# Performance work log

Measured on AMD Instinct MI355X. Metric: run time of the kernel, lower is better.

The kernel has to match this reference:

```python
import jax, jax.numpy as jnp
import numpy as np

N_NODES = 50000
E_DIM = 128
H_DIM = 256
OUT_DIM = 2
N_EDGES = 800000
NEG_SLOPE = 0.01  # nn.LeakyReLU default


def gcn_conv(x, W, b, src, dst, n):
    """PyG GCNConv: h = x @ W; add self-loops; sym-normalized scatter-add; + bias."""
    h = x @ W  # [N, H]
    loop = jnp.arange(n, dtype=src.dtype)
    s = jnp.concatenate([src, loop])
    d = jnp.concatenate([dst, loop])
    w = jnp.ones_like(s, dtype=h.dtype)
    deg = jax.ops.segment_sum(w, d, num_segments=n)  # in-degree incl. self-loop
    dis = jnp.where(deg > 0, jax.lax.rsqrt(deg), jnp.zeros_like(deg))
    norm = dis[s] * dis[d]  # [E+N]
    msg = h[s] * norm[:, None]  # gather + scale
    out = jax.ops.segment_sum(msg, d, num_segments=n)  # scatter-add to targets
    return out + b


def setup_inputs() -> dict:
    key = jax.random.key(0)
    ks = jax.random.split(key, 12)
    inp = {
        "mask_feature": jax.random.normal(ks[0], (N_NODES, E_DIM), jnp.float32),
        "feature": jax.random.normal(ks[1], (N_NODES, E_DIM), jnp.float32),
        "edge_index": jax.random.randint(ks[2], (2, N_EDGES), 0, N_NODES, jnp.int64 if jax.config.jax_enable_x64 else jnp.int32),
        "edge_type": jax.random.randint(ks[3], (N_EDGES,), 0, 2, jnp.int64 if jax.config.jax_enable_x64 else jnp.int32),
        # learned parameters
        "W_in": jax.random.normal(ks[4], (E_DIM, H_DIM), jnp.float32) * 0.05,
        "b_in": jnp.zeros((H_DIM,), jnp.float32),
        "Wg1": jax.random.normal(ks[5], (H_DIM, H_DIM), jnp.float32) * 0.05,
        "bg1": jnp.zeros((H_DIM,), jnp.float32),
        "Wg2": jax.random.normal(ks[6], (H_DIM, H_DIM), jnp.float32) * 0.05,
        "bg2": jnp.zeros((H_DIM,), jnp.float32),
        "W_out": jax.random.normal(ks[7], (H_DIM, OUT_DIM), jnp.float32) * 0.05,
        "b_out": jnp.zeros((OUT_DIM,), jnp.float32),
    }
    return inp


def reference(mask_feature, feature, edge_index, edge_type,
              W_in, b_in, Wg1, bg1, Wg2, bg2, W_out, b_out):
    src, dst = edge_index[0], edge_index[1]
    n = mask_feature.shape[0]
    # main branch
    x = jax.nn.leaky_relu(mask_feature @ W_in + b_in, NEG_SLOPE)
    x = gcn_conv(x, Wg1, bg1, src, dst, n)
    # dropout is identity at inference
    x = gcn_conv(x, Wg2, bg2, src, dst, n)
    x = x @ W_out + b_out  # [N, out_dim]
    # mask branch
    m = jax.nn.leaky_relu((feature - mask_feature) @ W_in + b_in, NEG_SLOPE)
    m = m @ W_out + b_out  # [N, out_dim]
    return x * m
```

## Files before the change

kernel.cpp:

```cpp
#include <hip/hip_runtime.h>


#define NEG_SLOPE 0.01f
constexpr int HD = 256;
constexpr int CHUNK = 4096;
constexpr int BSTRIDE = 8192;

typedef __bf16 bf16x8 __attribute__((ext_vector_type(8)));
typedef unsigned short u16x8 __attribute__((ext_vector_type(8)));
typedef float f32x4 __attribute__((ext_vector_type(4)));

#define MFMA16 __builtin_amdgcn_mfma_f32_16x16x32_bf16

__device__ inline void split1(float v, unsigned short& h, unsigned short& l) {
  unsigned u = __float_as_uint(v);
  unsigned hb = u & 0xFFFF0000u;
  float lf = v - __uint_as_float(hb);
  unsigned ul = __float_as_uint(lf);
  h = (unsigned short)(hb >> 16);
  l = (unsigned short)((ul + 0x7FFFu + ((ul >> 16) & 1u)) >> 16);
}

__global__ __launch_bounds__(256) void k_prep(
    const float* __restrict__ Win, u16x8* __restrict__ Wf,
    const float* __restrict__ Wg1, const float* __restrict__ Wg2,
    const float* __restrict__ Wo, const float* __restrict__ bg1,
    const float* __restrict__ bg2, const float* __restrict__ bo,
    float* __restrict__ wb, float* __restrict__ uv, int* __restrict__ cur) {
  __shared__ float wt[256][2];
  const int bid = blockIdx.x, tid = threadIdx.x;
  if (bid < 32) {
    int f = bid * 4 + (tid >> 6);
    int lane = tid & 63;
    int nt = f >> 3, ks = (f >> 1) & 3, hl = f & 1;
    int n = nt * 16 + (lane & 15);
    int k0 = ks * 32 + (lane >> 4) * 8;
    u16x8 outv;
    #pragma unroll
    for (int j = 0; j < 8; ++j) {
      unsigned short h, l;
      split1(Win[(size_t)(k0 + j) * HD + n], h, l);
      outv[j] = hl ? l : h;
    }
    Wf[f * 64 + lane] = outv;
  } else if (bid == 32) {
    int r = tid;
    float s0 = 0.f, s1 = 0.f;
    for (int k = 0; k < 256; ++k) {
      float w = Wg2[r * 256 + k];
      s0 = fmaf(w, Wo[k * 2 + 0], s0);
      s1 = fmaf(w, Wo[k * 2 + 1], s1);
    }
    wt[r][0] = s0; wt[r][1] = s1;
    __syncthreads();
    float b0 = 0.f, b1 = 0.f;
    for (int k = 0; k < 256; ++k) {
      float w = Wg1[r * 256 + k];
      b0 = fmaf(w, wt[k][0], b0);
      b1 = fmaf(w, wt[k][1], b1);
    }
    wb[r * 2 + 0] = b0; wb[r * 2 + 1] = b1;
    if (r < 2) {
      float u = 0.f, v = 0.f;
      for (int k = 0; k < 256; ++k) {
        u = fmaf(bg1[k], wt[k][r], u);
        v = fmaf(bg2[k], Wo[k * 2 + r], v);
      }
      uv[r] = u;
      uv[2 + r] = v + bo[r];
    }
  } else {
    cur[tid] = 0;
  }
}

__global__ __launch_bounds__(256) void k_scatter(
    const int* __restrict__ src, const int* __restrict__ dst,
    int* __restrict__ cur, unsigned* __restrict__ packed, int E) {
  __shared__ int bins[256], lstart[256], gbase[256], lcur[256];
  __shared__ int wsum[4];
  __shared__ unsigned sbuf[CHUNK];
  const int t = threadIdx.x, b = blockIdx.x;
  const int lane = t & 63, wid = t >> 6;
  bins[t] = 0;
  __syncthreads();
  const int e0 = b * CHUNK, e1 = min(e0 + CHUNK, E), m = e1 - e0;
  for (int e = e0 + t; e < e1; e += 256)
    atomicAdd(&bins[dst[e] >> 8], 1);
  __syncthreads();
  {
    int v = bins[t], incl = v;
    #pragma unroll
    for (int o = 1; o < 64; o <<= 1) {
      int tmp = __shfl_up(incl, o, 64);
      if (lane >= o) incl += tmp;
    }
    if (lane == 63) wsum[wid] = incl;
    __syncthreads();
    int woff = 0;
    for (int w = 0; w < wid; ++w) woff += wsum[w];
    int st = woff + incl - v;
    lstart[t] = st;
    lcur[t] = st;
    gbase[t] = v ? atomicAdd(&cur[t], v) : 0;
  }
  __syncthreads();
  for (int e = e0 + t; e < e1; e += 256) {
    int d = dst[e], s = src[e];
    int slot = atomicAdd(&lcur[d >> 8], 1);
    sbuf[slot] = ((unsigned)d << 16) | (unsigned)s;
  }
  __syncthreads();
  for (int i = t; i < m; i += 256) {
    unsigned pv = sbuf[i];
    int bin = pv >> 24;
    packed[(size_t)bin * BSTRIDE + gbase[bin] + (i - lstart[bin])] = pv;
  }
}

__global__ __launch_bounds__(256, 3) void k_main(
    const float* __restrict__ mf, const float* __restrict__ fe,
    const u16x8* __restrict__ Wf, const float* __restrict__ bi,
    const float* __restrict__ wb, const float* __restrict__ Wo,
    const float* __restrict__ bo, float4* __restrict__ q, float* __restrict__ Pm,
    const unsigned* __restrict__ packed, const int* __restrict__ cur,
    int* __restrict__ rp, int* __restrict__ csr, int N, int Gg) {
  __shared__ __align__(16) char smem[38912];
  const int tid = threadIdx.x;
  const int lane = tid & 63, wid = tid >> 6;

  if ((int)blockIdx.x < Gg) {
    u16x8*  sB  = (u16x8*)smem;
    float4* sE1 = (float4*)(smem + 32768);
    float2* sE2 = (float2*)(smem + 36864);
    sE1[tid] = make_float4(bi[tid], wb[2 * tid], wb[2 * tid + 1], 0.f);
    sE2[tid] = make_float2(Wo[2 * tid], Wo[2 * tid + 1]);

    const int base = blockIdx.x * 64 + wid * 16;
    int arow = base + (lane & 15);
    if (arow >= N) arow = N - 1;
    const int kb = (lane >> 4) * 8;
    const float* ap = mf + (size_t)arow * 128 + kb;
    const float* fp = fe + (size_t)arow * 128 + kb;

    bf16x8 ahi[4], alo[4], mhi[4], mlo[4];
    #pragma unroll
    for (int ks = 0; ks < 4; ++ks) {
      float x[8], y[8];
      *(float4*)&x[0] = *(const float4*)(ap + ks * 32);
      *(float4*)&x[4] = *(const float4*)(ap + ks * 32 + 4);
      *(float4*)&y[0] = *(const float4*)(fp + ks * 32);
      *(float4*)&y[4] = *(const float4*)(fp + ks * 32 + 4);
      u16x8 hA, lA, hM, lM;
      #pragma unroll
      for (int j = 0; j < 8; ++j) {
        unsigned short hh, ll;
        split1(x[j], hh, ll);        hA[j] = hh; lA[j] = ll;
        split1(y[j] - x[j], hh, ll); hM[j] = hh; lM[j] = ll;
      }
      ahi[ks] = __builtin_bit_cast(bf16x8, hA);
      alo[ks] = __builtin_bit_cast(bf16x8, lA);
      mhi[ks] = __builtin_bit_cast(bf16x8, hM);
      mlo[ks] = __builtin_bit_cast(bf16x8, lM);
    }

    float s0[4] = {}, s1[4] = {}, t0[4] = {}, t1[4] = {};
    #pragma unroll 1
    for (int g = 0; g < 4; ++g) {
      __syncthreads();
      #pragma unroll
      for (int i = 0; i < 8; ++i)
        sB[tid + i * 256] = Wf[g * 2048 + tid + i * 256];
      __syncthreads();
      #pragma unroll
      for (int ntl = 0; ntl < 4; ++ntl) {
        const int nt = g * 4 + ntl;
        f32x4 aM = {0, 0, 0, 0}, aK = {0, 0, 0, 0};
        #pragma unroll
        for (int ks = 0; ks < 4; ++ks) {
          bf16x8 bh = __builtin_bit_cast(bf16x8, sB[(ntl * 8 + ks * 2 + 0) * 64 + lane]);
          bf16x8 bl = __builtin_bit_cast(bf16x8, sB[(ntl * 8 + ks * 2 + 1) * 64 + lane]);
          aM = MFMA16(ahi[ks], bh, aM, 0, 0, 0);
          aM = MFMA16(alo[ks], bh, aM, 0, 0, 0);
          aM = MFMA16(ahi[ks], bl, aM, 0, 0, 0);
          aK = MFMA16(mhi[ks], bh, aK, 0, 0, 0);
          aK = MFMA16(mlo[ks], bh, aK, 0, 0, 0);
          aK = MFMA16(mhi[ks], bl, aK, 0, 0, 0);
        }
        const int col = nt * 16 + (lane & 15);
        const float4 e1 = sE1[col];
        const float2 e2 = sE2[col];
        #pragma unroll
        for (int r = 0; r < 4; ++r) {
          float a = aM[r] + e1.x; a = a > 0.f ? a : NEG_SLOPE * a;
          s0[r] = fmaf(a, e1.y, s0[r]); s1[r] = fmaf(a, e1.z, s1[r]);
          float m = aK[r] + e1.x; m = m > 0.f ? m : NEG_SLOPE * m;
          t0[r] = fmaf(m, e2.x, t0[r]); t1[r] = fmaf(m, e2.y, t1[r]);
        }
      }
    }

    #pragma unroll
    for (int o = 1; o < 16; o <<= 1) {
      #pragma unroll
      for (int r = 0; r < 4; ++r) {
        s0[r] += __shfl_xor(s0[r], o, 16); s1[r] += __shfl_xor(s1[r], o, 16);
        t0[r] += __shfl_xor(t0[r], o, 16); t1[r] += __shfl_xor(t1[r], o, 16);
      }
    }
    if ((lane & 15) == 0) {
      float bo0 = bo[0], bo1 = bo[1];
      #pragma unroll
      for (int r = 0; r < 4; ++r) {
        int row = base + (lane >> 4) * 4 + r;
        if (row < N) {
          float* qf = (float*)&q[row];
          qf[1] = s0[r];
          qf[2] = s1[r];
          Pm[row * 2 + 0] = t0[r] + bo0;
          Pm[row * 2 + 1] = t1[r] + bo1;
        }
      }
    }
    return;
  }

  int* cnt = (int*)smem;
  int* sc  = (int*)(smem + 1024);
  int* wsum = (int*)(smem + 2048);
  unsigned short* sbuf = (unsigned short*)(smem + 2064);
  const int t = tid;
  const int B = blockIdx.x - Gg;
  int tot = cur[t], incl = tot;
  #pragma unroll
  for (int o = 1; o < 64; o <<= 1) {
    int tmp = __shfl_up(incl, o, 64);
    if (lane >= o) incl += tmp;
  }
  if (lane == 63) wsum[wid] = incl;
  __syncthreads();
  int woff = 0;
  for (int w = 0; w < wid; ++w) woff += wsum[w];
  sc[t] = woff + incl - tot;
  __syncthreads();
  const int base = sc[B];
  const int ecnt = cur[B];
  const unsigned* pk = packed + (size_t)B * BSTRIDE;
  cnt[t] = 0;
  __syncthreads();
  for (int i = t; i < ecnt; i += 256)
    atomicAdd(&cnt[(pk[i] >> 16) & 0xFF], 1);
  __syncthreads();
  int v = cnt[t];
  incl = v;
  #pragma unroll
  for (int o = 1; o < 64; o <<= 1) {
    int tmp = __shfl_up(incl, o, 64);
    if (lane >= o) incl += tmp;
  }
  if (lane == 63) wsum[wid] = incl;
  __syncthreads();
  woff = 0;
  for (int w = 0; w < wid; ++w) woff += wsum[w];
  const int off = woff + incl - v;
  const int node = B * 256 + t;
  if (node < N) {
    rp[node] = base + off;
    ((float*)&q[node])[0] = rsqrtf((float)(v + 1));
  } else if (node == N) {
    rp[N] = base + off;
  }
  __syncthreads();
  cnt[t] = off;
  __syncthreads();
  for (int i = t; i < ecnt; i += 256) {
    unsigned pv = pk[i];
    int slot = atomicAdd(&cnt[(pv >> 16) & 0xFF], 1);
    sbuf[slot] = (unsigned short)(pv & 0xFFFFu);
  }
  __syncthreads();
  for (int i = t; i < ecnt; i += 256)
    csr[base + i] = (int)sbuf[i];
}

__global__ __launch_bounds__(256) void k_gather1(
    const int* __restrict__ rp, const int* __restrict__ csr,
    const float4* __restrict__ q, const float* __restrict__ uv,
    float* __restrict__ T2, int N) {
  int t = threadIdx.x;
  int n = blockIdx.x * 64 + (t >> 2);
  int l = t & 3;
  if (n >= N) return;
  int s0 = rp[n], s1 = rp[n + 1];
  float a0 = 0.f, a1 = 0.f;
  int j = s0 + l;
  for (; j + 12 < s1; j += 16) {
    int i0 = csr[j], i1 = csr[j + 4], i2 = csr[j + 8], i3 = csr[j + 12];
    float4 q0 = q[i0], q1 = q[i1], q2 = q[i2], q3 = q[i3];
    a0 = fmaf(q0.x, q0.y, a0); a1 = fmaf(q0.x, q0.z, a1);
    a0 = fmaf(q1.x, q1.y, a0); a1 = fmaf(q1.x, q1.z, a1);
    a0 = fmaf(q2.x, q2.y, a0); a1 = fmaf(q2.x, q2.z, a1);
    a0 = fmaf(q3.x, q3.y, a0); a1 = fmaf(q3.x, q3.z, a1);
  }
  for (; j < s1; j += 4) {
    float4 qa = q[csr[j]];
    a0 = fmaf(qa.x, qa.y, a0); a1 = fmaf(qa.x, qa.z, a1);
  }
  a0 += __shfl_xor(a0, 1, 4); a1 += __shfl_xor(a1, 1, 4);
  a0 += __shfl_xor(a0, 2, 4); a1 += __shfl_xor(a1, 2, 4);
  if (l == 0) {
    float4 qn = q[n];
    float d = qn.x;
    T2[n * 2 + 0] = d * (d * fmaf(d, qn.y, a0) + uv[0]);
    T2[n * 2 + 1] = d * (d * fmaf(d, qn.z, a1) + uv[1]);
  }
}

__global__ __launch_bounds__(256) void k_gather2(
    const int* __restrict__ rp, const int* __restrict__ csr,
    const float* __restrict__ T2, const float4* __restrict__ q,
    const float* __restrict__ uv, const float* __restrict__ Pm,
    float* __restrict__ out, int N) {
  int t = threadIdx.x;
  int n = blockIdx.x * 64 + (t >> 2);
  int l = t & 3;
  if (n >= N) return;
  int s0 = rp[n], s1 = rp[n + 1];
  float a0 = 0.f, a1 = 0.f;
  int j = s0 + l;
  for (; j + 12 < s1; j += 16) {
    int i0 = csr[j], i1 = csr[j + 4], i2 = csr[j + 8], i3 = csr[j + 12];
    float2 v0 = *(const float2*)&T2[i0 * 2];
    float2 v1 = *(const float2*)&T2[i1 * 2];
    float2 v2 = *(const float2*)&T2[i2 * 2];
    float2 v3 = *(const float2*)&T2[i3 * 2];
    a0 += (v0.x + v1.x) + (v2.x + v3.x);
    a1 += (v0.y + v1.y) + (v2.y + v3.y);
  }
  for (; j < s1; j += 4) {
    float2 va = *(const float2*)&T2[csr[j] * 2];
    a0 += va.x; a1 += va.y;
  }
  a0 += __shfl_xor(a0, 1, 4); a1 += __shfl_xor(a1, 1, 4);
  a0 += __shfl_xor(a0, 2, 4); a1 += __shfl_xor(a1, 2, 4);
  if (l == 0) {
    float d = q[n].x;
    float2 tv = *(const float2*)&T2[n * 2];
    float z0 = d * (tv.x + a0) + uv[2];
    float z1 = d * (tv.y + a1) + uv[3];
    out[n * 2 + 0] = z0 * Pm[n * 2 + 0];
    out[n * 2 + 1] = z1 * Pm[n * 2 + 1];
  }
}

extern "C" void kernel_launch(void* const* d_in, const int* in_sizes, int n_in,
                              void* d_out, int out_size, void* d_ws, size_t ws_size,
                              hipStream_t stream) {
  const float* mf  = (const float*)d_in[0];
  const float* fe  = (const float*)d_in[1];
  const int*   ei  = (const int*)d_in[2];
  const float* Win = (const float*)d_in[4];
  const float* bin = (const float*)d_in[5];
  const float* Wg1 = (const float*)d_in[6];
  const float* bg1 = (const float*)d_in[7];
  const float* Wg2 = (const float*)d_in[8];
  const float* bg2 = (const float*)d_in[9];
  const float* Wo  = (const float*)d_in[10];
  const float* bo  = (const float*)d_in[11];
  float* out = (float*)d_out;

  const int ED = 128;
  const int N = in_sizes[0] / ED;
  const int E = in_sizes[3];
  const int* src = ei;
  const int* dst = ei + E;

  char* ws = (char*)d_ws;
  size_t off = 0;
  auto carve = [&](size_t bytes) {
    char* p = ws + off;
    off += (bytes + 255) & ~(size_t)255;
    return p;
  };
  int*      cur    = (int*)carve(256 * 4);
  unsigned* packed = (unsigned*)carve((size_t)256 * BSTRIDE * 4);
  int*      csr    = (int*)carve((size_t)E * 4);
  int*      rp     = (int*)carve((size_t)(N + 1) * 4);
  float4*   q      = (float4*)carve((size_t)N * 16);
  float*    T2     = (float*)carve((size_t)N * 2 * 4);
  float*    Pm     = (float*)carve((size_t)N * 2 * 4);
  float*    wb     = (float*)carve((size_t)HD * 2 * 4);
  float*    uv     = (float*)carve(4 * 4);
  u16x8*    Wf     = (u16x8*)carve((size_t)128 * 64 * 16);
  (void)ws_size; (void)n_in; (void)out_size;

  const int NB  = (E + CHUNK - 1) / CHUNK;
  const int NP2 = (N + 255) / 256;
  const int Gg  = (N + 63) / 64;
  const int Gt  = (N + 63) / 64;

  k_prep<<<34, 256, 0, stream>>>(Win, Wf, Wg1, Wg2, Wo, bg1, bg2, bo, wb, uv, cur);
  k_scatter<<<NB, 256, 0, stream>>>(src, dst, cur, packed, E);
  k_main<<<Gg + NP2, 256, 0, stream>>>(mf, fe, Wf, bin, wb, Wo, bo, q, Pm,
                                       packed, cur, rp, csr, N, Gg);
  k_gather1<<<Gt, 256, 0, stream>>>(rp, csr, q, uv, T2, N);
  k_gather2<<<Gt, 256, 0, stream>>>(rp, csr, T2, q, uv, Pm, out, N);
}
```

Baseline: 89.54 us.

## Stage A tiles through swizzled LDS with coalesced loads; stream W fragments from global

The input rows are now loaded with coalesced float4 reads across the block, split into bf16 hi/lo pieces, and written to a swizzled LDS layout. Each wave then reads its MFMA A fragments from that layout. The weight fragments are no longer staged through LDS with block barriers. Each lane loads them straight from global (L2-cached) memory into registers, double-buffered one n-tile ahead. LDS usage grows to about 70KB and launch bounds drop to 2 blocks per CU, which trades occupancy for better load coalescing and fewer syncs.

```diff
diff --git a/kernel.cpp b/kernel.cpp
--- a/kernel.cpp
+++ b/kernel.cpp
@@ -19,6 +19,11 @@
   unsigned ul = __float_as_uint(lf);
   h = (unsigned short)(hb >> 16);
   l = (unsigned short)((ul + 0x7FFFu + ((ul >> 16) & 1u)) >> 16);
+}
+
+__device__ inline uint2 pack4(const unsigned short* s) {
+  return make_uint2((unsigned)s[0] | ((unsigned)s[1] << 16),
+                    (unsigned)s[2] | ((unsigned)s[3] << 16));
 }
 
 __global__ __launch_bounds__(256) void k_prep(
@@ -118,107 +123,126 @@
   }
 }
 
-__global__ __launch_bounds__(256, 3) void k_main(
+__global__ __launch_bounds__(256, 2) void k_main(
     const float* __restrict__ mf, const float* __restrict__ fe,
     const u16x8* __restrict__ Wf, const float* __restrict__ bi,
     const float* __restrict__ wb, const float* __restrict__ Wo,
     const float* __restrict__ bo, float4* __restrict__ q, float* __restrict__ Pm,
     const unsigned* __restrict__ packed, const int* __restrict__ cur,
     int* __restrict__ rp, int* __restrict__ csr, int N, int Gg) {
-  __shared__ __align__(16) char smem[38912];
+  __shared__ __align__(16) char smem[71680];
   const int tid = threadIdx.x;
   const int lane = tid & 63, wid = tid >> 6;
 
   if ((int)blockIdx.x < Gg) {
-    u16x8*  sB  = (u16x8*)smem;
-    float4* sE1 = (float4*)(smem + 32768);
-    float2* sE2 = (float2*)(smem + 36864);
+    char* sA = smem;
+    float4* sE1 = (float4*)(smem + 65536);
+    float2* sE2 = (float2*)(smem + 69632);
     sE1[tid] = make_float4(bi[tid], wb[2 * tid], wb[2 * tid + 1], 0.f);
     sE2[tid] = make_float2(Wo[2 * tid], Wo[2 * tid + 1]);
 
-    const int base = blockIdx.x * 64 + wid * 16;
-    int arow = base + (lane & 15);
-    if (arow >= N) arow = N - 1;
-    const int kb = (lane >> 4) * 8;
-    const float* ap = mf + (size_t)arow * 128 + kb;
-    const float* fp = fe + (size_t)arow * 128 + kb;
-
-    bf16x8 ahi[4], alo[4], mhi[4], mlo[4];
+    const int gb = blockIdx.x * 64;
+    #pragma unroll
+    for (int p = 0; p < 8; ++p) {
+      int i = p * 256 + tid;
+      int row = i >> 5, c = i & 31;
+      int gr = gb + row;
+      if (gr >= N) gr = N - 1;
+      float4 xm = ((const float4*)mf)[(size_t)gr * 32 + c];
+      float4 xf = ((const float4*)fe)[(size_t)gr * 32 + c];
+      unsigned short mh[4], ml[4], kh[4], kl[4];
+      float xs[4] = {xm.x, xm.y, xm.z, xm.w};
+      float ys[4] = {xf.x - xm.x, xf.y - xm.y, xf.z - xm.z, xf.w - xm.w};
+      #pragma unroll
+      for (int j = 0; j < 4; ++j) {
+        split1(xs[j], mh[j], ml[j]);
+        split1(ys[j], kh[j], kl[j]);
+      }
+      int c4 = c * 4;
+      int panel = row >> 4, r = row & 15;
+      int ks = c4 >> 5, kbg = (c4 >> 3) & 3, j0 = c4 & 7;
+      int a = panel * 4096 + ks * 1024 + (kbg * 16 + r) * 16 + j0 * 2;
+      a ^= (kbg << 4) ^ ((ks & 1) << 6);
+      *(uint2*)(sA + a)         = pack4(mh);
+      *(uint2*)(sA + 16384 + a) = pack4(ml);
+      *(uint2*)(sA + 32768 + a) = pack4(kh);
+      *(uint2*)(sA + 49152 + a) = pack4(kl);
+    }
+    __syncthreads();
+
+    bf16x8 Ah[4], Al[4], Kh[4], Kl[4];
     #pragma unroll
     for (int ks = 0; ks < 4; ++ks) {
-      float x[8], y[8];
-      *(float4*)&x[0] = *(const float4*)(ap + ks * 32);
-      *(float4*)&x[4] = *(const float4*)(ap + ks * 32 + 4);
-      *(float4*)&y[0] = *(const float4*)(fp + ks * 32);
-      *(float4*)&y[4] = *(const float4*)(fp + ks * 32 + 4);
-      u16x8 hA, lA, hM, lM;
-      #pragma unroll
-      for (int j = 0; j < 8; ++j) {
-        unsigned short hh, ll;
-        split1(x[j], hh, ll);        hA[j] = hh; lA[j] = ll;
-        split1(y[j] - x[j], hh, ll); hM[j] = hh; lM[j] = ll;
-      }
-      ahi[ks] = __builtin_bit_cast(bf16x8, hA);
-      alo[ks] = __builtin_bit_cast(bf16x8, lA);
-      mhi[ks] = __builtin_bit_cast(bf16x8, hM);
-      mlo[ks] = __builtin_bit_cast(bf16x8, lM);
-    }
-
-    float s0[4] = {}, s1[4] = {}, t0[4] = {}, t1[4] = {};
+      int a = wid * 4096 + ks * 1024 + lane * 16;
+      a ^= ((lane >> 4) << 4) ^ ((ks & 1) << 6);
+      Ah[ks] = *(const bf16x8*)(sA + a);
+      Al[ks] = *(const bf16x8*)(sA + 16384 + a);
+      Kh[ks] = *(const bf16x8*)(sA + 32768 + a);
+      Kl[ks] = *(const bf16x8*)(sA + 49152 + a);
+    }
+
+    const u16x8* wp = Wf + lane;
+    float s0[4] = {}, s1[4] = {}, t0v[4] = {}, t1v[4] = {};
+    u16x8 bA[8], bB[8];
+    #pragma unroll
+    for (int f = 0; f < 8; ++f) bA[f] = wp[f * 64];
+
+    auto COMPUTE = [&](const u16x8* b, int nt) {
+      f32x4 aM = {0, 0, 0, 0}, aK = {0, 0, 0, 0};
+      #pragma unroll
+      for (int ks = 0; ks < 4; ++ks) {
+        bf16x8 bh = __builtin_bit_cast(bf16x8, b[ks * 2 + 0]);
+        bf16x8 bl = __builtin_bit_cast(bf16x8, b[ks * 2 + 1]);
+        aM = MFMA16(Ah[ks], bh, aM, 0, 0, 0);
+        aM = MFMA16(Al[ks], bh, aM, 0, 0, 0);
+        aM = MFMA16(Ah[ks], bl, aM, 0, 0, 0);
+        aK = MFMA16(Kh[ks], bh, aK, 0, 0, 0);
+        aK = MFMA16(Kl[ks], bh, aK, 0, 0, 0);
+        aK = MFMA16(Kh[ks], bl, aK, 0, 0, 0);
+      }
+      const int col = nt * 16 + (lane & 15);
+      const float4 e1 = sE1[col];
+      const float2 e2 = sE2[col];
+      #pragma unroll
+      for (int r = 0; r < 4; ++r) {
+        float a = aM[r] + e1.x; a = a > 0.f ? a : NEG_SLOPE * a;
+        s0[r] = fmaf(a, e1.y, s0[r]); s1[r] = fmaf(a, e1.z, s1[r]);
+        float m = aK[r] + e1.x; m = m > 0.f ? m : NEG_SLOPE * m;
+        t0v[r] = fmaf(m, e2.x, t0v[r]); t1v[r] = fmaf(m, e2.y, t1v[r]);
+      }
+    };
+
     #pragma unroll 1
-    for (int g = 0; g < 4; ++g) {
-      __syncthreads();
-      #pragma unroll
-      for (int i = 0; i < 8; ++i)
-        sB[tid + i * 256] = Wf[g * 2048 + tid + i * 256];
-      __syncthreads();
-      #pragma unroll
-      for (int ntl = 0; ntl < 4; ++ntl) {
-        const int nt = g * 4 + ntl;
-        f32x4 aM = {0, 0, 0, 0}, aK = {0, 0, 0, 0};
+    for (int nt = 0; nt < 16; nt += 2) {
+      #pragma unroll
+      for (int f = 0; f < 8; ++f) bB[f] = wp[((nt + 1) * 8 + f) * 64];
+      COMPUTE(bA, nt);
+      if (nt + 2 < 16) {
         #pragma unroll
-        for (int ks = 0; ks < 4; ++ks) {
-          bf16x8 bh = __builtin_bit_cast(bf16x8, sB[(ntl * 8 + ks * 2 + 0) * 64 + lane]);
-          bf16x8 bl = __builtin_bit_cast(bf16x8, sB[(ntl * 8 + ks * 2 + 1) * 64 + lane]);
-          aM = MFMA16(ahi[ks], bh, aM, 0, 0, 0);
-          aM = MFMA16(alo[ks], bh, aM, 0, 0, 0);
-          aM = MFMA16(ahi[ks], bl, aM, 0, 0, 0);
-          aK = MFMA16(mhi[ks], bh, aK, 0, 0, 0);
-          aK = MFMA16(mlo[ks], bh, aK, 0, 0, 0);
-          aK = MFMA16(mhi[ks], bl, aK, 0, 0, 0);
-        }
-        const int col = nt * 16 + (lane & 15);
-        const float4 e1 = sE1[col];
-        const float2 e2 = sE2[col];
-        #pragma unroll
-        for (int r = 0; r < 4; ++r) {
-          float a = aM[r] + e1.x; a = a > 0.f ? a : NEG_SLOPE * a;
-          s0[r] = fmaf(a, e1.y, s0[r]); s1[r] = fmaf(a, e1.z, s1[r]);
-          float m = aK[r] + e1.x; m = m > 0.f ? m : NEG_SLOPE * m;
-          t0[r] = fmaf(m, e2.x, t0[r]); t1[r] = fmaf(m, e2.y, t1[r]);
-        }
-      }
+        for (int f = 0; f < 8; ++f) bA[f] = wp[((nt + 2) * 8 + f) * 64];
+      }
+      COMPUTE(bB, nt + 1);
     }
 
     #pragma unroll
     for (int o = 1; o < 16; o <<= 1) {
       #pragma unroll
       for (int r = 0; r < 4; ++r) {
-        s0[r] += __shfl_xor(s0[r], o, 16); s1[r] += __shfl_xor(s1[r], o, 16);
-        t0[r] += __shfl_xor(t0[r], o, 16); t1[r] += __shfl_xor(t1[r], o, 16);
+        s0[r] += __shfl_xor(s0[r], o, 16);  s1[r] += __shfl_xor(s1[r], o, 16);
+        t0v[r] += __shfl_xor(t0v[r], o, 16); t1v[r] += __shfl_xor(t1v[r], o, 16);
       }
     }
     if ((lane & 15) == 0) {
       float bo0 = bo[0], bo1 = bo[1];
       #pragma unroll
       for (int r = 0; r < 4; ++r) {
-        int row = base + (lane >> 4) * 4 + r;
+        int row = gb + wid * 16 + (lane >> 4) * 4 + r;
         if (row < N) {
           float* qf = (float*)&q[row];
           qf[1] = s0[r];
           qf[2] = s1[r];
-          Pm[row * 2 + 0] = t0[r] + bo0;
-          Pm[row * 2 + 1] = t1[r] + bo1;
+          Pm[row * 2 + 0] = t0v[r] + bo0;
+          Pm[row * 2 + 1] = t1v[r] + bo1;
         }
       }
     }
```

After: 88.92 us. About the same (-0.7%).

## Stream weight fragments from global into double-buffered registers instead of LDS

Applied to the files above, without the earlier changes.

Drops the per-group LDS staging of the bf16 weight fragments and their block-wide barriers. Each lane now loads its B fragments straight from global (L2-cached) memory into two register buffers, prefetching the next column tile while computing the current one. The split-precision MFMAs are spread over three independent accumulators per branch to shorten dependency chains, and LDS use shrinks, which may allow more resident blocks. The cost is more VGPRs and repeated global loads of the weights by every wave.

```diff
diff --git a/kernel.cpp b/kernel.cpp
--- a/kernel.cpp
+++ b/kernel.cpp
@@ -125,25 +125,25 @@
     const float* __restrict__ bo, float4* __restrict__ q, float* __restrict__ Pm,
     const unsigned* __restrict__ packed, const int* __restrict__ cur,
     int* __restrict__ rp, int* __restrict__ csr, int N, int Gg) {
-  __shared__ __align__(16) char smem[38912];
+  __shared__ __align__(16) char smem[18560];
   const int tid = threadIdx.x;
   const int lane = tid & 63, wid = tid >> 6;
 
   if ((int)blockIdx.x < Gg) {
-    u16x8*  sB  = (u16x8*)smem;
-    float4* sE1 = (float4*)(smem + 32768);
-    float2* sE2 = (float2*)(smem + 36864);
+    float4* sE1 = (float4*)smem;
+    float2* sE2 = (float2*)(smem + 4096);
     sE1[tid] = make_float4(bi[tid], wb[2 * tid], wb[2 * tid + 1], 0.f);
     sE2[tid] = make_float2(Wo[2 * tid], Wo[2 * tid + 1]);
 
-    const int base = blockIdx.x * 64 + wid * 16;
+    const int gb = blockIdx.x * 64;
+    const int base = gb + wid * 16;
     int arow = base + (lane & 15);
     if (arow >= N) arow = N - 1;
     const int kb = (lane >> 4) * 8;
     const float* ap = mf + (size_t)arow * 128 + kb;
     const float* fp = fe + (size_t)arow * 128 + kb;
 
-    bf16x8 ahi[4], alo[4], mhi[4], mlo[4];
+    bf16x8 Ah[4], Al[4], Kh[4], Kl[4];
     #pragma unroll
     for (int ks = 0; ks < 4; ++ks) {
       float x[8], y[8];
@@ -158,54 +158,65 @@
         split1(x[j], hh, ll);        hA[j] = hh; lA[j] = ll;
         split1(y[j] - x[j], hh, ll); hM[j] = hh; lM[j] = ll;
       }
-      ahi[ks] = __builtin_bit_cast(bf16x8, hA);
-      alo[ks] = __builtin_bit_cast(bf16x8, lA);
-      mhi[ks] = __builtin_bit_cast(bf16x8, hM);
-      mlo[ks] = __builtin_bit_cast(bf16x8, lM);
-    }
-
-    float s0[4] = {}, s1[4] = {}, t0[4] = {}, t1[4] = {};
+      Ah[ks] = __builtin_bit_cast(bf16x8, hA);
+      Al[ks] = __builtin_bit_cast(bf16x8, lA);
+      Kh[ks] = __builtin_bit_cast(bf16x8, hM);
+      Kl[ks] = __builtin_bit_cast(bf16x8, lM);
+    }
+    __syncthreads();
+
+    const u16x8* wp = Wf + lane;
+    float s0[4] = {}, s1[4] = {}, t0v[4] = {}, t1v[4] = {};
+    u16x8 bA[8], bB[8];
+    #pragma unroll
+    for (int f = 0; f < 8; ++f) bA[f] = wp[f * 64];
+
+    auto COMPUTE = [&](const u16x8* b, int nt) {
+      f32x4 a0 = {0,0,0,0}, a1 = {0,0,0,0}, a2 = {0,0,0,0};
+      f32x4 k0 = {0,0,0,0}, k1 = {0,0,0,0}, k2 = {0,0,0,0};
+      #pragma unroll
+      for (int ks = 0; ks < 4; ++ks) {
+        bf16x8 bh = __builtin_bit_cast(bf16x8, b[ks * 2 + 0]);
+        bf16x8 bl = __builtin_bit_cast(bf16x8, b[ks * 2 + 1]);
+        a0 = MFMA16(Ah[ks], bh, a0, 0, 0, 0);
+        a1 = MFMA16(Al[ks], bh, a1, 0, 0, 0);
+        a2 = MFMA16(Ah[ks], bl, a2, 0, 0, 0);
+        k0 = MFMA16(Kh[ks], bh, k0, 0, 0, 0);
+        k1 = MFMA16(Kl[ks], bh, k1, 0, 0, 0);
+        k2 = MFMA16(Kh[ks], bl, k2, 0, 0, 0);
+      }
+      const int col = nt * 16 + (lane & 15);
+      const float4 e1 = sE1[col];
+      const float2 e2 = sE2[col];
+      #pragma unroll
+      for (int r = 0; r < 4; ++r) {
+        float a = (a0[r] + a1[r]) + (a2[r] + e1.x);
+        a = a > 0.f ? a : NEG_SLOPE * a;
+        s0[r] = fmaf(a, e1.y, s0[r]); s1[r] = fmaf(a, e1.z, s1[r]);
+        float m = (k0[r] + k1[r]) + (k2[r] + e1.x);
+        m = m > 0.f ? m : NEG_SLOPE * m;
+        t0v[r] = fmaf(m, e2.x, t0v[r]); t1v[r] = fmaf(m, e2.y, t1v[r]);
+      }
+    };
+
     #pragma unroll 1
-    for (int g = 0; g < 4; ++g) {
-      __syncthreads();
-      #pragma unroll
-      for (int i = 0; i < 8; ++i)
-        sB[tid + i * 256] = Wf[g * 2048 + tid + i * 256];
-      __syncthreads();
-      #pragma unroll
-      for (int ntl = 0; ntl < 4; ++ntl) {
-        const int nt = g * 4 + ntl;
-        f32x4 aM = {0, 0, 0, 0}, aK = {0, 0, 0, 0};
+    for (int nt = 0; nt < 16; nt += 2) {
+      #pragma unroll
+      for (int f = 0; f < 8; ++f) bB[f] = wp[((nt + 1) * 8 + f) * 64];
+      COMPUTE(bA, nt);
+      if (nt + 2 < 16) {
         #pragma unroll
-        for (int ks = 0; ks < 4; ++ks) {
-          bf16x8 bh = __builtin_bit_cast(bf16x8, sB[(ntl * 8 + ks * 2 + 0) * 64 + lane]);
-          bf16x8 bl = __builtin_bit_cast(bf16x8, sB[(ntl * 8 + ks * 2 + 1) * 64 + lane]);
-          aM = MFMA16(ahi[ks], bh, aM, 0, 0, 0);
-          aM = MFMA16(alo[ks], bh, aM, 0, 0, 0);
-          aM = MFMA16(ahi[ks], bl, aM, 0, 0, 0);
-          aK = MFMA16(mhi[ks], bh, aK, 0, 0, 0);
-          aK = MFMA16(mlo[ks], bh, aK, 0, 0, 0);
-          aK = MFMA16(mhi[ks], bl, aK, 0, 0, 0);
-        }
-        const int col = nt * 16 + (lane & 15);
-        const float4 e1 = sE1[col];
-        const float2 e2 = sE2[col];
-        #pragma unroll
-        for (int r = 0; r < 4; ++r) {
-          float a = aM[r] + e1.x; a = a > 0.f ? a : NEG_SLOPE * a;
-          s0[r] = fmaf(a, e1.y, s0[r]); s1[r] = fmaf(a, e1.z, s1[r]);
-          float m = aK[r] + e1.x; m = m > 0.f ? m : NEG_SLOPE * m;
-          t0[r] = fmaf(m, e2.x, t0[r]); t1[r] = fmaf(m, e2.y, t1[r]);
-        }
-      }
+        for (int f = 0; f < 8; ++f) bA[f] = wp[((nt + 2) * 8 + f) * 64];
+      }
+      COMPUTE(bB, nt + 1);
     }
 
     #pragma unroll
     for (int o = 1; o < 16; o <<= 1) {
       #pragma unroll
       for (int r = 0; r < 4; ++r) {
-        s0[r] += __shfl_xor(s0[r], o, 16); s1[r] += __shfl_xor(s1[r], o, 16);
-        t0[r] += __shfl_xor(t0[r], o, 16); t1[r] += __shfl_xor(t1[r], o, 16);
+        s0[r] += __shfl_xor(s0[r], o, 16);  s1[r] += __shfl_xor(s1[r], o, 16);
+        t0v[r] += __shfl_xor(t0v[r], o, 16); t1v[r] += __shfl_xor(t1v[r], o, 16);
       }
     }
     if ((lane & 15) == 0) {
@@ -217,8 +228,8 @@
           float* qf = (float*)&q[row];
           qf[1] = s0[r];
           qf[2] = s1[r];
-          Pm[row * 2 + 0] = t0[r] + bo0;
-          Pm[row * 2 + 1] = t1[r] + bo1;
+          Pm[row * 2 + 0] = t0v[r] + bo0;
+          Pm[row * 2 + 1] = t1v[r] + bo1;
         }
       }
     }
```

Measured after the change: 125.2 us. +39.9%, slower.
